# Performance work log

Hardware: AMD Instinct MI355X
Metric: run time of the kernel (lower is better)

The kernel has to match this reference:

```python
import jax, jax.numpy as jnp
import numpy as np

N_EMB = 1024
N_HEADS = 16
HS = N_EMB // N_HEADS  # 64
BASE = 10000.0


def _rope_cache(T):
    # theta uses dim = n_emb (as in the source), sliced to hs//2 frequencies
    i = jnp.arange(HS // 2, dtype=jnp.float32)
    theta = BASE ** (-2.0 * i / N_EMB)            # [hs/2]
    pos = jnp.arange(T, dtype=jnp.float32)        # [T]
    ang = pos[:, None] * theta[None, :]           # [T, hs/2]
    return jnp.cos(ang), jnp.sin(ang)


def _apply_rope(x, cos, sin):
    # x: [B, T, nh, hs]; rotate consecutive pairs along hs
    b, t, nh, hs = x.shape
    xr = x.reshape(b, t, nh, hs // 2, 2)
    c = cos[None, :, None, :]
    s = sin[None, :, None, :]
    r0 = xr[..., 0] * c - xr[..., 1] * s
    r1 = xr[..., 1] * c + xr[..., 0] * s
    return jnp.stack([r0, r1], axis=-1).reshape(b, t, nh, hs)


def setup_inputs() -> dict:
    key = jax.random.key(0)
    k1, k2, k3, k4 = jax.random.split(key, 4)
    B, T = 2, 2048
    w_std = 0.02
    x = jax.random.normal(k1, (B, T, N_EMB), jnp.float32)
    Wq = jax.random.normal(k2, (N_EMB, N_EMB), jnp.float32) * w_std
    Wk = jax.random.normal(k3, (N_EMB, N_EMB), jnp.float32) * w_std
    Wv = jax.random.normal(k4, (N_EMB, N_EMB), jnp.float32) * w_std
    return {"x": x, "Wq": Wq, "Wk": Wk, "Wv": Wv}


def reference(x, Wq, Wk, Wv):
    B, T, C = x.shape
    # nn.Linear(bias=False): y = x @ W.T
    q = (x @ Wq.T).reshape(B, T, N_HEADS, HS)
    k = (x @ Wk.T).reshape(B, T, N_HEADS, HS)
    v = (x @ Wv.T).reshape(B, T, N_HEADS, HS)
    cos, sin = _rope_cache(T)
    q = _apply_rope(q, cos, sin)
    k = _apply_rope(k, cos, sin)
    # scale uses C (n_emb), as in the source (not head_size)
    wei = jnp.einsum('bqhd,bkhd->bhqk', q, k) * (C ** -0.5)  # [B, nh, T, T]
    mask = jnp.tril(jnp.ones((T, T), dtype=bool))
    wei = jnp.where(mask[None, None], wei, -jnp.inf)
    wei = jax.nn.softmax(wei, axis=-1)
    # dropout is identity in eval mode
    out = jnp.einsum('bhqk,bkhd->bqhd', wei, v).reshape(B, T, C)
    return out
```

## Files before the change

### kernel.cpp

```cpp
#include <hip/hip_runtime.h>
#include <stdint.h>

typedef unsigned short u16;
typedef __bf16 bf16x8 __attribute__((ext_vector_type(8)));
typedef unsigned short u16x8 __attribute__((ext_vector_type(8)));
typedef float f32x4 __attribute__((ext_vector_type(4)));
typedef uint32_t u32v4 __attribute__((ext_vector_type(4)));

#define LOG2E 1.4426950408889634f

typedef const __attribute__((address_space(1))) uint32_t as1_u32;
typedef __attribute__((address_space(3))) uint32_t as3_u32;

__device__ __forceinline__ u16 f2bf(float f) {
  union { float f; uint32_t i; } v; v.f = f;
  uint32_t r = (v.i + 0x7fffu + ((v.i >> 16) & 1u)) >> 16;
  return (u16)r;
}
__device__ __forceinline__ float bf2f(u16 u) {
  union { uint32_t i; float f; } v; v.i = ((uint32_t)u) << 16; return v.f;
}

__device__ __forceinline__ void gld_lds16(const void* g, void* l) {
  as1_u32* gp = (as1_u32*)((uintptr_t)g);
  as3_u32* lp = (as3_u32*)(uint32_t)(uintptr_t)(l);
  __builtin_amdgcn_global_load_lds(gp, lp, 16, 0, 0);
}

__device__ __forceinline__ float fast_exp2(float x) {
  float r;
  asm("v_exp_f32 %0, %1" : "=v"(r) : "v"(x));
  return r;
}

__global__ __launch_bounds__(256) void f32_to_bf16(
    const float* __restrict__ x, const float* __restrict__ wq,
    const float* __restrict__ wk, const float* __restrict__ wv,
    u16* __restrict__ xc, u16* __restrict__ wqc,
    u16* __restrict__ wkc, u16* __restrict__ wvc) {
  const int z = blockIdx.y;
  const float* src = z == 0 ? x : (z == 1 ? wq : (z == 2 ? wk : wv));
  u16* dst = z == 0 ? xc : (z == 1 ? wqc : (z == 2 ? wkc : wvc));
  const int n = z == 0 ? (1 << 22) : (1 << 20);

  const int idx = (blockIdx.x * 256 + (int)threadIdx.x) * 8;
  if (idx >= n) return;
  const f32x4 a = *(const f32x4*)&src[idx];
  const f32x4 b = *(const f32x4*)&src[idx + 4];
  u16x8 o;
#pragma unroll
  for (int j = 0; j < 4; j++) { o[j] = f2bf(a[j]); o[j + 4] = f2bf(b[j]); }
  *(u16x8*)&dst[idx] = o;
}

__global__ __launch_bounds__(256) void qkv_gemm(
    const u16* __restrict__ xc, const u16* __restrict__ wqc,
    const u16* __restrict__ wkc, const u16* __restrict__ wvc,
    u16* __restrict__ qo, u16* __restrict__ ko, u16* __restrict__ vt) {
  __shared__ __align__(16) u16 As[128 * 64];
  __shared__ __align__(16) u16 Bs[128 * 64];

  const int tid = threadIdx.x;
  const int lane = tid & 63;
  const int w = tid >> 6;
  const int wm = w >> 1, wn = w & 1;
  const int quad = lane >> 4, m16 = lane & 15;

  const int id    = (int)blockIdx.x;
  const int xcd   = id & 7;
  const int local = id >> 3;
  const int by    = xcd * 4 + (local & 3);
  const int rest  = local >> 2;
  const int which = rest % 3;
  const int bx    = rest / 3;

  const u16* __restrict__ Ap;
  const u16* __restrict__ Bp;
  int m0, n0;
  if (which == 2) {
    Ap = wvc; Bp = xc;
    m0 = bx * 128;
    n0 = by * 128;
  } else {
    Ap = xc; Bp = which == 0 ? wqc : wkc;
    m0 = by * 128;
    n0 = bx * 128;
  }

  const f32x4 z4 = {0.f, 0.f, 0.f, 0.f};
  f32x4 acc[4][4];
#pragma unroll
  for (int i = 0; i < 4; i++)
#pragma unroll
    for (int j = 0; j < 4; j++) acc[i][j] = z4;

  const int lrow = lane >> 3;
  const int scol = ((lane & 7) ^ (lrow & 7)) * 8;
  const int srowA = m0 + w * 32 + lrow;
  const int srowB = n0 + w * 32 + lrow;
  const int rsw = m16 & 7;

  for (int k0 = 0; k0 < 1024; k0 += 64) {
    __syncthreads();
#pragma unroll
    for (int j = 0; j < 4; j++) {
      gld_lds16(&Ap[(size_t)(srowA + j * 8) * 1024 + k0 + scol],
                &As[(w * 32 + j * 8) * 64]);
      gld_lds16(&Bp[(size_t)(srowB + j * 8) * 1024 + k0 + scol],
                &Bs[(w * 32 + j * 8) * 64]);
    }
    __syncthreads();

#pragma unroll
    for (int kk = 0; kk < 2; kk++) {
      bf16x8 af[4], bfr[4];
#pragma unroll
      for (int t = 0; t < 4; t++) {
        af[t] = *(const bf16x8*)
            &As[(wm * 64 + t * 16 + m16) * 64 + (((kk * 4 + quad) ^ rsw) * 8)];
        bfr[t] = *(const bf16x8*)
            &Bs[(wn * 64 + t * 16 + m16) * 64 + (((kk * 4 + quad) ^ rsw) * 8)];
      }
#pragma unroll
      for (int mt = 0; mt < 4; mt++)
#pragma unroll
        for (int nt = 0; nt < 4; nt++)
          acc[mt][nt] = __builtin_amdgcn_mfma_f32_16x16x32_bf16(
              af[mt], bfr[nt], acc[mt][nt], 0, 0, 0);
    }
  }

  if (which < 2) {
    u16* __restrict__ out = which == 0 ? qo : ko;
#pragma unroll
    for (int mt = 0; mt < 4; mt++) {
      const int row = m0 + wm * 64 + mt * 16 + quad * 4;
#pragma unroll
      for (int nt = 0; nt < 4; nt++) {
        const int n = n0 + wn * 64 + nt * 16 + m16;
        f32x4 a = acc[mt][nt];
#pragma unroll
        for (int r = 0; r < 4; r++)
          out[(size_t)(row + r) * 1024 + n] = f2bf(a[r]);
      }
    }
  } else {
    const int m16p = (m16 & 3) | ((m16 & 4) << 1) | ((m16 & 8) >> 1);
#pragma unroll
    for (int mt = 0; mt < 4; mt++) {
      const int row = m0 + wm * 64 + mt * 16 + quad * 4;
#pragma unroll
      for (int nt = 0; nt < 4; nt++) {
        const int n = n0 + wn * 64 + nt * 16 + m16p;
        f32x4 a = acc[mt][nt];
#pragma unroll
        for (int r = 0; r < 4; r++)
          vt[(size_t)(row + r) * 4096 + n] = f2bf(a[r]);
      }
    }
  }
}

__global__ __launch_bounds__(256) void rope_inplace(u16* __restrict__ qb,
                                                    u16* __restrict__ kb) {
  u16* buf = blockIdx.y == 0 ? qb : kb;
  const int p = blockIdx.x * 256 + (int)threadIdx.x;
  const int e0 = p * 8;
  const int row = e0 >> 10;
  const int col0 = e0 & 1023;
  const int t = row & 2047;
  const float tf = (float)t;

  u16x8 d = *(const u16x8*)&buf[(size_t)row * 1024 + col0];
  u16x8 o;
#pragma unroll
  for (int j = 0; j < 4; j++) {
    const int i = ((col0 & 63) >> 1) + j;
    const float th = fast_exp2(-(float)i * 0.02595256324130752f);
    const float rev = tf * th * 0.15915494309189535f;
    float fr, s, c;
    asm("v_fract_f32 %0, %1" : "=v"(fr) : "v"(rev));
    asm("v_sin_f32 %0, %1" : "=v"(s) : "v"(fr));
    asm("v_cos_f32 %0, %1" : "=v"(c) : "v"(fr));
    const float a0 = bf2f(d[2 * j]), a1 = bf2f(d[2 * j + 1]);
    o[2 * j]     = f2bf(a0 * c - a1 * s);
    o[2 * j + 1] = f2bf(a1 * c + a0 * s);
  }
  *(u16x8*)&buf[(size_t)row * 1024 + col0] = o;
}

__global__ __launch_bounds__(256, 2) void flash_attn(
    const u16* __restrict__ qg, const u16* __restrict__ kg,
    const u16* __restrict__ vt, float* __restrict__ out) {
  __shared__ __align__(16) u16 Ks[2][128 * 72];
  __shared__ __align__(16) u16 Vs[2][64 * 136];

  const int tid = threadIdx.x, lane = tid & 63, w = tid >> 6;
  const int quad = lane >> 4, m16 = lane & 15;

  const int id   = (int)blockIdx.x;
  const int X    = id & 7;
  const int rem  = id >> 3;
  const int s    = rem & 1;
  const int vloc = (rem >> 1) & 3;
  const int kk_  = rem >> 3;
  const int Q    = s ? 15 - kk_ : kk_;
  const int v    = X * 4 + vloc;
  const int h    = v & 15;
  const int b    = v >> 4;

  const size_t base  = (size_t)b * 2048 * 1024 + (size_t)h * 64;
  const size_t vbase = (size_t)(h * 64) * 4096 + (size_t)b * 2048;
  const float SC = 0.03125f * LOG2E;
  const f32x4 z4 = {0.f, 0.f, 0.f, 0.f};
  const int srow = tid >> 2, sc = (tid & 3) * 16;

  union { u16x8 u; bf16x8 f; } ones;
#pragma unroll
  for (int k = 0; k < 8; k++) ones.u[k] = 0x3F80;

  const int q0 = Q * 128;
  const int nr = Q + 1;

  const u16* qsA = &qg[base + (size_t)(q0 + w * 32 + m16) * 1024 + quad * 8];
  const bf16x8 qfA0 = *(const bf16x8*)qsA;
  const bf16x8 qfA1 = *(const bf16x8*)(qsA + 32);
  const u16* qsB = qsA + (size_t)16 * 1024;
  const bf16x8 qfB0 = *(const bf16x8*)qsB;
  const bf16x8 qfB1 = *(const bf16x8*)(qsB + 32);

  u16x8 kr0, kr1, kr2, kr3, vr0, vr1, vr2, vr3;
  {
    const u16* ks = &kg[base + (size_t)srow * 1024 + sc];
    kr0 = *(const u16x8*)ks; kr1 = *(const u16x8*)(ks + 8);
    const u16* ks2 = ks + (size_t)64 * 1024;
    kr2 = *(const u16x8*)ks2; kr3 = *(const u16x8*)(ks2 + 8);
    const u16* vs = &vt[vbase + (size_t)srow * 4096 + sc];
    vr0 = *(const u16x8*)vs; vr1 = *(const u16x8*)(vs + 8);
    vr2 = *(const u16x8*)(vs + 64); vr3 = *(const u16x8*)(vs + 72);
  }

  f32x4 lA = z4, lB = z4;
  f32x4 OA[4], OB[4];
#pragma unroll
  for (int d = 0; d < 4; d++) { OA[d] = z4; OB[d] = z4; }

  const int qrowA = q0 + w * 32 + quad * 4;
  const int qcolA = q0 + w * 32 + m16;

  int p = 0;
  for (int rr = 0; rr < nr; ++rr) {
    const int k0 = rr * 128;
    u16* ksp = &Ks[p][0];
    u16* vsp = &Vs[p][0];
    *(u16x8*)&ksp[srow * 72 + sc] = kr0;
    *(u16x8*)&ksp[srow * 72 + sc + 8] = kr1;
    *(u16x8*)&ksp[(64 + srow) * 72 + sc] = kr2;
    *(u16x8*)&ksp[(64 + srow) * 72 + sc + 8] = kr3;
    *(u16x8*)&vsp[srow * 136 + sc] = vr0;
    *(u16x8*)&vsp[srow * 136 + sc + 8] = vr1;
    *(u16x8*)&vsp[srow * 136 + 64 + sc] = vr2;
    *(u16x8*)&vsp[srow * 136 + 64 + sc + 8] = vr3;
    if (rr + 1 < nr) {
      const u16* ks = &kg[base + (size_t)(k0 + 128 + srow) * 1024 + sc];
      kr0 = *(const u16x8*)ks; kr1 = *(const u16x8*)(ks + 8);
      const u16* ks2 = ks + (size_t)64 * 1024;
      kr2 = *(const u16x8*)ks2; kr3 = *(const u16x8*)(ks2 + 8);
      const u16* vs = &vt[vbase + (size_t)srow * 4096 + k0 + 128 + sc];
      vr0 = *(const u16x8*)vs; vr1 = *(const u16x8*)(vs + 8);
      vr2 = *(const u16x8*)(vs + 64); vr3 = *(const u16x8*)(vs + 72);
    }
    __syncthreads();

    f32x4 SA[8], SB[8];
#pragma unroll
    for (int nt = 0; nt < 8; nt++) {
      const bf16x8 kf0 = *(const bf16x8*)&ksp[(nt * 16 + m16) * 72 + quad * 8];
      const bf16x8 kf1 =
          *(const bf16x8*)&ksp[(nt * 16 + m16) * 72 + 32 + quad * 8];
      SA[nt] = __builtin_amdgcn_mfma_f32_16x16x32_bf16(kf0, qfA0, z4, 0, 0, 0);
      SA[nt] = __builtin_amdgcn_mfma_f32_16x16x32_bf16(kf1, qfA1, SA[nt], 0, 0, 0);
      SB[nt] = __builtin_amdgcn_mfma_f32_16x16x32_bf16(kf0, qfB0, z4, 0, 0, 0);
      SB[nt] = __builtin_amdgcn_mfma_f32_16x16x32_bf16(kf1, qfB1, SB[nt], 0, 0, 0);
    }

    const bool lastr = (rr == nr - 1);

    union { u32v4 u; bf16x8 f; } PA[4], PB[4];
    {
      uint32_t W[16];
#pragma unroll
      for (int nt = 0; nt < 8; nt++) {
        float pe[4];
#pragma unroll
        for (int r = 0; r < 4; r++) {
          float e = fast_exp2(SA[nt][r] * SC);
          const int key = k0 + nt * 16 + quad * 4 + r;
          if (lastr && key > qcolA) e = 0.f;
          pe[r] = e;
        }
        uint32_t w0, w1;
        asm("v_cvt_pk_bf16_f32 %0, %1, %2" : "=v"(w0) : "v"(pe[0]), "v"(pe[1]));
        asm("v_cvt_pk_bf16_f32 %0, %1, %2" : "=v"(w1) : "v"(pe[2]), "v"(pe[3]));
        W[2 * nt] = w0; W[2 * nt + 1] = w1;
      }
#pragma unroll
      for (int ks = 0; ks < 4; ks++) {
        uint32_t a0 = W[4 * ks], b0 = W[4 * ks + 2];
        uint32_t a1 = W[4 * ks + 1], b1 = W[4 * ks + 3];
        asm("v_permlane32_swap_b32 %0, %1" : "+v"(a0), "+v"(b0));
        asm("v_permlane32_swap_b32 %0, %1" : "+v"(a1), "+v"(b1));
        PA[ks].u = (u32v4){a0, a1, b0, b1};
      }
    }
    {
      const int qcolB = qcolA + 16;
      uint32_t W[16];
#pragma unroll
      for (int nt = 0; nt < 8; nt++) {
        float pe[4];
#pragma unroll
        for (int r = 0; r < 4; r++) {
          float e = fast_exp2(SB[nt][r] * SC);
          const int key = k0 + nt * 16 + quad * 4 + r;
          if (lastr && key > qcolB) e = 0.f;
          pe[r] = e;
        }
        uint32_t w0, w1;
        asm("v_cvt_pk_bf16_f32 %0, %1, %2" : "=v"(w0) : "v"(pe[0]), "v"(pe[1]));
        asm("v_cvt_pk_bf16_f32 %0, %1, %2" : "=v"(w1) : "v"(pe[2]), "v"(pe[3]));
        W[2 * nt] = w0; W[2 * nt + 1] = w1;
      }
#pragma unroll
      for (int ks = 0; ks < 4; ks++) {
        uint32_t a0 = W[4 * ks], b0 = W[4 * ks + 2];
        uint32_t a1 = W[4 * ks + 1], b1 = W[4 * ks + 3];
        asm("v_permlane32_swap_b32 %0, %1" : "+v"(a0), "+v"(b0));
        asm("v_permlane32_swap_b32 %0, %1" : "+v"(a1), "+v"(b1));
        PB[ks].u = (u32v4){a0, a1, b0, b1};
      }
    }

#pragma unroll
    for (int ks = 0; ks < 4; ks++) {
      lA = __builtin_amdgcn_mfma_f32_16x16x32_bf16(PA[ks].f, ones.f, lA, 0, 0, 0);
      lB = __builtin_amdgcn_mfma_f32_16x16x32_bf16(PB[ks].f, ones.f, lB, 0, 0, 0);
    }

#pragma unroll
    for (int dt = 0; dt < 4; dt++) {
#pragma unroll
      for (int ks = 0; ks < 4; ks++) {
        const bf16x8 vf =
            *(const bf16x8*)&vsp[(dt * 16 + m16) * 136 + ks * 32 + quad * 8];
        OA[dt] = __builtin_amdgcn_mfma_f32_16x16x32_bf16(PA[ks].f, vf, OA[dt],
                                                         0, 0, 0);
        OB[dt] = __builtin_amdgcn_mfma_f32_16x16x32_bf16(PB[ks].f, vf, OB[dt],
                                                         0, 0, 0);
      }
    }
    p ^= 1;
  }

  float invA[4], invB[4];
#pragma unroll
  for (int r = 0; r < 4; r++) { invA[r] = 1.0f / lA[r]; invB[r] = 1.0f / lB[r]; }

#pragma unroll
  for (int dt = 0; dt < 4; dt++)
#pragma unroll
    for (int r = 0; r < 4; r++) {
      out[base + (size_t)(qrowA + r) * 1024 + dt * 16 + m16] =
          OA[dt][r] * invA[r];
      out[base + (size_t)(qrowA + 16 + r) * 1024 + dt * 16 + m16] =
          OB[dt][r] * invB[r];
    }
}

extern "C" void kernel_launch(void* const* d_in, const int* in_sizes, int n_in,
                              void* d_out, int out_size, void* d_ws, size_t ws_size,
                              hipStream_t stream) {
  const float* x  = (const float*)d_in[0];
  const float* Wq = (const float*)d_in[1];
  const float* Wk = (const float*)d_in[2];
  const float* Wv = (const float*)d_in[3];
  u16* qb  = (u16*)d_ws;
  u16* kb  = qb  + (size_t)4096 * 1024;
  u16* vtw = kb  + (size_t)4096 * 1024;
  u16* xc  = vtw + (size_t)4096 * 1024;
  u16* wqc = xc  + (size_t)4096 * 1024;
  u16* wkc = wqc + (size_t)1024 * 1024;
  u16* wvc = wkc + (size_t)1024 * 1024;

  f32_to_bf16<<<dim3(2048, 4), 256, 0, stream>>>(x, Wq, Wk, Wv,
                                                 xc, wqc, wkc, wvc);
  qkv_gemm<<<dim3(768, 1, 1), 256, 0, stream>>>(xc, wqc, wkc, wvc,
                                                qb, kb, vtw);
  rope_inplace<<<dim3(2048, 2), 256, 0, stream>>>(qb, kb);
  flash_attn<<<dim3(512, 1, 1), 256, 0, stream>>>(qb, kb, vtw, (float*)d_out);
}
```

Baseline: 152.7 us.

## Split causal attention KV range across blocks with atomic accumulation and normalize pass

Splits each query tile's key range into chunks of up to four 128-key tiles, so the grid grows from 512 to 1280 blocks with more balanced per-block work. Each block atomically adds its unnormalized partial output and row-sum into the output buffer and a row-sum buffer. Both buffers are zeroed in the conversion kernel, and a new kernel divides by the row sums at the end. This relies on no running max being subtracted in the exp, so partial results can be summed directly. It adds atomic traffic, one extra launch and an extra read/write pass over the output.

Result: slower. 180.4 us (+18.1%).

```diff
diff --git a/kernel.cpp b/kernel.cpp
--- a/kernel.cpp
+++ b/kernel.cpp
@@ -37,13 +37,22 @@
     const float* __restrict__ x, const float* __restrict__ wq,
     const float* __restrict__ wk, const float* __restrict__ wv,
     u16* __restrict__ xc, u16* __restrict__ wqc,
-    u16* __restrict__ wkc, u16* __restrict__ wvc) {
+    u16* __restrict__ wkc, u16* __restrict__ wvc,
+    float* __restrict__ oz, float* __restrict__ lz) {
   const int z = blockIdx.y;
+  const int idx = (blockIdx.x * 256 + (int)threadIdx.x) * 8;
+  if (z >= 4) {
+    const f32x4 zz = {0.f, 0.f, 0.f, 0.f};
+    if (z == 4) {
+      *(f32x4*)&oz[idx] = zz; *(f32x4*)&oz[idx + 4] = zz;
+    } else if (idx < 65536) {
+      *(f32x4*)&lz[idx] = zz; *(f32x4*)&lz[idx + 4] = zz;
+    }
+    return;
+  }
   const float* src = z == 0 ? x : (z == 1 ? wq : (z == 2 ? wk : wv));
   u16* dst = z == 0 ? xc : (z == 1 ? wqc : (z == 2 ? wkc : wvc));
   const int n = z == 0 ? (1 << 22) : (1 << 20);
-
-  const int idx = (blockIdx.x * 256 + (int)threadIdx.x) * 8;
   if (idx >= n) return;
   const f32x4 a = *(const f32x4*)&src[idx];
   const f32x4 b = *(const f32x4*)&src[idx + 4];
@@ -191,7 +200,8 @@
 
 __global__ __launch_bounds__(256, 2) void flash_attn(
     const u16* __restrict__ qg, const u16* __restrict__ kg,
-    const u16* __restrict__ vt, float* __restrict__ out) {
+    const u16* __restrict__ vt, float* __restrict__ out,
+    float* __restrict__ lacc) {
   __shared__ __align__(16) u16 Ks[2][128 * 72];
   __shared__ __align__(16) u16 Vs[2][64 * 136];
 
@@ -201,10 +211,13 @@
   const int id   = (int)blockIdx.x;
   const int X    = id & 7;
   const int rem  = id >> 3;
-  const int s    = rem & 1;
-  const int vloc = (rem >> 1) & 3;
-  const int kk_  = rem >> 3;
-  const int Q    = s ? 15 - kk_ : kk_;
+  const int vloc = rem & 3;
+  const int item = 39 - (rem >> 2);
+  int Q, cc;
+  if (item < 4)        { Q = item;                 cc = 0; }
+  else if (item < 12)  { const int t = item - 4;  Q = 4 + (t >> 1); cc = t & 1; }
+  else if (item < 24)  { const int t = item - 12; Q = 8 + t / 3;    cc = t % 3; }
+  else                 { const int t = item - 24; Q = 12 + (t >> 2); cc = t & 3; }
   const int v    = X * 4 + vloc;
   const int h    = v & 15;
   const int b    = v >> 4;
@@ -220,7 +233,8 @@
   for (int k = 0; k < 8; k++) ones.u[k] = 0x3F80;
 
   const int q0 = Q * 128;
-  const int nr = Q + 1;
+  const int r0 = cc * 4;
+  const int r1 = min(r0 + 4, Q + 1);
 
   const u16* qsA = &qg[base + (size_t)(q0 + w * 32 + m16) * 1024 + quad * 8];
   const bf16x8 qfA0 = *(const bf16x8*)qsA;
@@ -231,11 +245,12 @@
 
   u16x8 kr0, kr1, kr2, kr3, vr0, vr1, vr2, vr3;
   {
-    const u16* ks = &kg[base + (size_t)srow * 1024 + sc];
+    const int kb0 = r0 * 128;
+    const u16* ks = &kg[base + (size_t)(kb0 + srow) * 1024 + sc];
     kr0 = *(const u16x8*)ks; kr1 = *(const u16x8*)(ks + 8);
     const u16* ks2 = ks + (size_t)64 * 1024;
     kr2 = *(const u16x8*)ks2; kr3 = *(const u16x8*)(ks2 + 8);
-    const u16* vs = &vt[vbase + (size_t)srow * 4096 + sc];
+    const u16* vs = &vt[vbase + (size_t)srow * 4096 + kb0 + sc];
     vr0 = *(const u16x8*)vs; vr1 = *(const u16x8*)(vs + 8);
     vr2 = *(const u16x8*)(vs + 64); vr3 = *(const u16x8*)(vs + 72);
   }
@@ -249,7 +264,7 @@
   const int qcolA = q0 + w * 32 + m16;
 
   int p = 0;
-  for (int rr = 0; rr < nr; ++rr) {
+  for (int rr = r0; rr < r1; ++rr) {
     const int k0 = rr * 128;
     u16* ksp = &Ks[p][0];
     u16* vsp = &Vs[p][0];
@@ -261,7 +276,7 @@
     *(u16x8*)&vsp[srow * 136 + sc + 8] = vr1;
     *(u16x8*)&vsp[srow * 136 + 64 + sc] = vr2;
     *(u16x8*)&vsp[srow * 136 + 64 + sc + 8] = vr3;
-    if (rr + 1 < nr) {
+    if (rr + 1 < r1) {
       const u16* ks = &kg[base + (size_t)(k0 + 128 + srow) * 1024 + sc];
       kr0 = *(const u16x8*)ks; kr1 = *(const u16x8*)(ks + 8);
       const u16* ks2 = ks + (size_t)64 * 1024;
@@ -284,7 +299,7 @@
       SB[nt] = __builtin_amdgcn_mfma_f32_16x16x32_bf16(kf1, qfB1, SB[nt], 0, 0, 0);
     }
 
-    const bool lastr = (rr == nr - 1);
+    const bool lastr = (rr == Q);
 
     union { u32v4 u; bf16x8 f; } PA[4], PB[4];
     {
@@ -362,19 +377,34 @@
     p ^= 1;
   }
 
-  float invA[4], invB[4];
-#pragma unroll
-  for (int r = 0; r < 4; r++) { invA[r] = 1.0f / lA[r]; invB[r] = 1.0f / lB[r]; }
-
 #pragma unroll
   for (int dt = 0; dt < 4; dt++)
 #pragma unroll
     for (int r = 0; r < 4; r++) {
-      out[base + (size_t)(qrowA + r) * 1024 + dt * 16 + m16] =
-          OA[dt][r] * invA[r];
-      out[base + (size_t)(qrowA + 16 + r) * 1024 + dt * 16 + m16] =
-          OB[dt][r] * invB[r];
-    }
+      atomicAdd(&out[base + (size_t)(qrowA + r) * 1024 + dt * 16 + m16],
+                OA[dt][r]);
+      atomicAdd(&out[base + (size_t)(qrowA + 16 + r) * 1024 + dt * 16 + m16],
+                OB[dt][r]);
+    }
+  if (m16 == 0) {
+#pragma unroll
+    for (int r = 0; r < 4; r++) {
+      atomicAdd(&lacc[((size_t)b * 2048 + qrowA + r) * 16 + h], lA[r]);
+      atomicAdd(&lacc[((size_t)b * 2048 + qrowA + 16 + r) * 16 + h], lB[r]);
+    }
+  }
+}
+
+__global__ __launch_bounds__(256) void attn_norm(float* __restrict__ out,
+                                                 const float* __restrict__ lacc) {
+  const int e0 = (blockIdx.x * 256 + (int)threadIdx.x) * 8;
+  const float inv = 1.0f / lacc[e0 >> 6];
+  f32x4 a = *(const f32x4*)&out[e0];
+  f32x4 b = *(const f32x4*)&out[e0 + 4];
+#pragma unroll
+  for (int j = 0; j < 4; j++) { a[j] *= inv; b[j] *= inv; }
+  *(f32x4*)&out[e0] = a;
+  *(f32x4*)&out[e0 + 4] = b;
 }
 
 extern "C" void kernel_launch(void* const* d_in, const int* in_sizes, int n_in,
@@ -391,11 +421,15 @@
   u16* wqc = xc  + (size_t)4096 * 1024;
   u16* wkc = wqc + (size_t)1024 * 1024;
   u16* wvc = wkc + (size_t)1024 * 1024;
-
-  f32_to_bf16<<<dim3(2048, 4), 256, 0, stream>>>(x, Wq, Wk, Wv,
-                                                 xc, wqc, wkc, wvc);
+  float* lacc = (float*)(wvc + (size_t)1024 * 1024);
+  float* outf = (float*)d_out;
+
+  f32_to_bf16<<<dim3(2048, 6), 256, 0, stream>>>(x, Wq, Wk, Wv,
+                                                 xc, wqc, wkc, wvc,
+                                                 outf, lacc);
   qkv_gemm<<<dim3(768, 1, 1), 256, 0, stream>>>(xc, wqc, wkc, wvc,
                                                 qb, kb, vtw);
   rope_inplace<<<dim3(2048, 2), 256, 0, stream>>>(qb, kb);
-  flash_attn<<<dim3(512, 1, 1), 256, 0, stream>>>(qb, kb, vtw, (float*)d_out);
-}
+  flash_attn<<<dim3(1280, 1, 1), 256, 0, stream>>>(qb, kb, vtw, outf, lacc);
+  attn_norm<<<dim3(2048, 1, 1), 256, 0, stream>>>(outf, lacc);
+}
```
